# Optimization experiments

Hardware: AMD Instinct MI355X
Metric: run time of the kernel (lower is better)

Reference implementation:

```python
import jax, jax.numpy as jnp
import numpy as np

EPS = 1e-5

def layer_norm(x, g, b):
    m = jnp.mean(x, axis=-1, keepdims=True)
    v = jnp.var(x, axis=-1, keepdims=True)
    return (x - m) / jnp.sqrt(v + EPS) * g + b


def setup_inputs() -> dict:
    key = jax.random.key(0)
    ks = jax.random.split(key, 12)
    B, L, D = 4, 4096, 512
    DF = 2 * D  # dim * dim_ff_scale
    inp = {
        "x": jax.random.normal(ks[0], (B, L, D), dtype=jnp.float32),
        "hidden_real": jax.random.normal(ks[1], (B, D), dtype=jnp.float32),
        "hidden_imag": jax.random.normal(ks[2], (B, D), dtype=jnp.float32),
        # SpiralConv complex params (real/imag parts), as torch.randn cfloat
        "phazor_re": jax.random.normal(ks[3], (D,), dtype=jnp.float32),
        "phazor_im": jax.random.normal(ks[4], (D,), dtype=jnp.float32),
        "pinit_re": jax.random.normal(ks[5], (D,), dtype=jnp.float32),
        "pinit_im": jax.random.normal(ks[6], (D,), dtype=jnp.float32),
        # shared LayerNorm params
        "ln_g": jnp.ones((D,), dtype=jnp.float32),
        "ln_b": jnp.zeros((D,), dtype=jnp.float32),
        # FFN params
        "w1": jax.random.normal(ks[7], (D, DF), dtype=jnp.float32) * (1.0 / np.sqrt(D)),
        "b1": jnp.zeros((DF,), dtype=jnp.float32),
        "w2": jax.random.normal(ks[8], (DF, D), dtype=jnp.float32) * (1.0 / np.sqrt(DF)),
        "b2": jnp.zeros((D,), dtype=jnp.float32),
    }
    return inp


def reference(x, hidden_real, hidden_imag, phazor_re, phazor_im,
              pinit_re, pinit_im, ln_g, ln_b, w1, b1, w2, b2):
    B, L, D = x.shape
    p = jax.lax.complex(phazor_re, phazor_im)
    pinit = jax.lax.complex(pinit_re, pinit_im)
    hidden_last = jax.lax.complex(hidden_real, hidden_imag)

    # phazor = p/|p| * exp(-|p|)  (unit direction, decaying magnitude)
    absp = jnp.abs(p)
    phazor = p / absp * jnp.exp(-absp)

    # phazor_progression[t, d] = phazor[d] ** t
    t = jnp.arange(L, dtype=jnp.float32)
    prog = jnp.exp(t[:, None] * jnp.log(phazor)[None, :])  # [L, D] complex
    filt = prog * pinit[None, :]                            # [L, D]

    x_res = x
    xn = layer_norm(x, ln_g, ln_b)

    # FFT long convolution along sequence, zero-padded to 2L (linear conv)
    filt_fft = jnp.fft.fft(filt, n=2 * L, axis=0)           # [2L, D]
    x_fft = jnp.fft.fft(xn, n=2 * L, axis=1)                # [B, 2L, D]
    conv = jnp.fft.ifft(filt_fft[None, :, :] * x_fft, axis=1)[:, :L, :]

    hidden = conv + hidden_last[:, None, :] * prog[None, :, :] * phazor[None, None, :]

    y = hidden.real + x_res
    yn = layer_norm(y, ln_g, ln_b)
    h = yn @ w1 + b1
    h = h * jax.nn.sigmoid(h)  # SiLU; dropout=0 (eval) is identity
    out = h @ w2 + b2 + y
    return out, hidden
```

## Files before the change

kernel.cpp:

```cpp
#include <hip/hip_runtime.h>
#include <hip/hip_bf16.h>
#include <math.h>

#define BB 4
#define LL 4096
#define DD 512
#define DF 1024
#define CHUNKS 64
#define LC 64
#define HALF_ROWS 8192

typedef __bf16 bf16x8 __attribute__((ext_vector_type(8)));
typedef float f32x4 __attribute__((ext_vector_type(4)));

__device__ inline void get_phazor(const float* __restrict__ pre, const float* __restrict__ pim,
                                  int d, float& ar, float& ai) {
    float pr = pre[d], pi = pim[d];
    float ab = sqrtf(pr * pr + pi * pi);
    float sc = expf(-ab) / ab;
    ar = pr * sc;
    ai = pi * sc;
}

__global__ __launch_bounds__(256) void k_wt(const float* __restrict__ w1, const float* __restrict__ w2,
                                            __bf16* __restrict__ w1t, __bf16* __restrict__ w2t) {
    __shared__ float tile[32][33];
    const float* src;
    __bf16* dst;
    int R, C;
    if (blockIdx.y == 0) { src = w1; dst = w1t; R = DD; C = DF; }
    else                 { src = w2; dst = w2t; R = DF; C = DD; }
    int ntx = C / 32;
    int c0 = (blockIdx.x % ntx) * 32, r0 = (blockIdx.x / ntx) * 32;
    int tx = threadIdx.x & 31, ty = threadIdx.x >> 5;
#pragma unroll
    for (int i = 0; i < 32; i += 8)
        tile[ty + i][tx] = src[(size_t)(r0 + ty + i) * C + c0 + tx];
    __syncthreads();
#pragma unroll
    for (int i = 0; i < 32; i += 8)
        dst[(size_t)(c0 + ty + i) * R + r0 + tx] = (__bf16)tile[tx][ty + i];
}

__global__ __launch_bounds__(256) void k_xstats(const float* __restrict__ x, float* __restrict__ xstats) {
    int wave = threadIdx.x >> 6, lane = threadIdx.x & 63;
    size_t row = (size_t)blockIdx.x * 4 + wave;
    const float4* xr = reinterpret_cast<const float4*>(x + row * DD) + lane * 2;
    float4 a = xr[0], b = xr[1];
    float s = a.x + a.y + a.z + a.w + b.x + b.y + b.z + b.w;
    float q = a.x * a.x + a.y * a.y + a.z * a.z + a.w * a.w +
              b.x * b.x + b.y * b.y + b.z * b.z + b.w * b.w;
#pragma unroll
    for (int off = 32; off; off >>= 1) {
        s += __shfl_down(s, off);
        q += __shfl_down(q, off);
    }
    if (lane == 0) {
        float m = s * (1.0f / DD);
        float v = q * (1.0f / DD) - m * m;
        xstats[row * 2 + 0] = m;
        xstats[row * 2 + 1] = rsqrtf(v + 1e-5f);
    }
}

__global__ __launch_bounds__(512) void k_scan_partial(
    const float* __restrict__ x, const float* __restrict__ xstats,
    const float* __restrict__ pre, const float* __restrict__ pim,
    const float* __restrict__ pinr, const float* __restrict__ pini,
    const float* __restrict__ g, const float* __restrict__ bvec,
    float* __restrict__ carry) {
    int d = threadIdx.x;
    int c = blockIdx.x % CHUNKS, b = blockIdx.x / CHUNKS;
    float ar, ai;
    get_phazor(pre, pim, d, ar, ai);
    float pr = pinr[d], pi = pini[d];
    float gd = g[d], bd = bvec[d];
    float hr = 0.f, hi = 0.f;
    int l0 = c * LC;
    const float* xp = x + ((size_t)b * LL + l0) * DD + d;
    const float* st = xstats + ((size_t)b * LL + l0) * 2;
    for (int i = 0; i < LC; i++) {
        float m = st[2 * i], r = st[2 * i + 1];
        float xn = (xp[(size_t)i * DD] - m) * r * gd + bd;
        float ur = pr * xn, ui = pi * xn;
        float t = ar * hr - ai * hi + ur;
        hi = ar * hi + ai * hr + ui;
        hr = t;
    }
    size_t idx = ((size_t)blockIdx.x * DD + d) * 2;
    carry[idx] = hr;
    carry[idx + 1] = hi;
}

__global__ __launch_bounds__(512) void k_chunk_scan(
    const float* __restrict__ hr0, const float* __restrict__ hi0,
    const float* __restrict__ pre, const float* __restrict__ pim,
    const float* __restrict__ carry, float* __restrict__ carry_in) {
    int d = threadIdx.x, b = blockIdx.x;
    float ar, ai;
    get_phazor(pre, pim, d, ar, ai);
    float sr = ar, si = ai;
#pragma unroll
    for (int i = 0; i < 6; i++) {
        float t = sr * sr - si * si;
        si = 2.f * sr * si;
        sr = t;
    }
    float cr = hr0[b * DD + d], ci = hi0[b * DD + d];
    for (int k = 0; k < CHUNKS; k++) {
        size_t idx = (((size_t)b * CHUNKS + k) * DD + d) * 2;
        carry_in[idx] = cr;
        carry_in[idx + 1] = ci;
        float tr = carry[idx], ti = carry[idx + 1];
        float t = sr * cr - si * ci + tr;
        ci = sr * ci + si * cr + ti;
        cr = t;
    }
}

template <int MODE>
__global__ __launch_bounds__(512) void k_scan_out(
    const float* __restrict__ x, const float* __restrict__ xstats,
    const float* __restrict__ pre, const float* __restrict__ pim,
    const float* __restrict__ pinr, const float* __restrict__ pini,
    const float* __restrict__ g, const float* __restrict__ bvec,
    const float* __restrict__ carry_in,
    float* __restrict__ out_y, float* __restrict__ hid) {
    int d = threadIdx.x;
    int c = blockIdx.x % CHUNKS, b = blockIdx.x / CHUNKS;
    float ar, ai;
    get_phazor(pre, pim, d, ar, ai);
    float pr = pinr[d], pi = pini[d];
    float gd = g[d], bd = bvec[d];
    size_t cidx = ((size_t)blockIdx.x * DD + d) * 2;
    float hr = carry_in[cidx], hi = carry_in[cidx + 1];
    int l0 = c * LC;
    const float* xp = x + ((size_t)b * LL + l0) * DD + d;
    const float* st = xstats + ((size_t)b * LL + l0) * 2;
    for (int i = 0; i < LC; i++) {
        float m = st[2 * i], r = st[2 * i + 1];
        float xv = xp[(size_t)i * DD];
        float xn = (xv - m) * r * gd + bd;
        float ur = pr * xn, ui = pi * xn;
        float t = ar * hr - ai * hi + ur;
        hi = ar * hi + ai * hr + ui;
        hr = t;
        size_t row = (size_t)b * LL + l0 + i;
        if constexpr (MODE == 0) {
            out_y[row * DD + d] = hr + xv;
        } else if constexpr (MODE == 1) {
            hid[row * DD + d] = hr;
        } else if constexpr (MODE == 2) {
            reinterpret_cast<float2*>(hid)[row * DD + d] = make_float2(hr, hi);
        } else {
            out_y[row * DD + d] = hr + xv;
            hid[row * DD + d] = hr;
        }
    }
}

__global__ __launch_bounds__(256) void k_ynorm(const float* __restrict__ y,
                                               const float* __restrict__ g, const float* __restrict__ bvec,
                                               __bf16* __restrict__ yn) {
    int wave = threadIdx.x >> 6, lane = threadIdx.x & 63;
    size_t row = (size_t)blockIdx.x * 4 + wave;
    const float4* yr = reinterpret_cast<const float4*>(y + row * DD) + lane * 2;
    float4 a = yr[0], b = yr[1];
    float s = a.x + a.y + a.z + a.w + b.x + b.y + b.z + b.w;
    float q = a.x * a.x + a.y * a.y + a.z * a.z + a.w * a.w +
              b.x * b.x + b.y * b.y + b.z * b.z + b.w * b.w;
#pragma unroll
    for (int off = 32; off; off >>= 1) {
        s += __shfl_xor(s, off);
        q += __shfl_xor(q, off);
    }
    float m = s * (1.0f / DD);
    float r = rsqrtf(q * (1.0f / DD) - m * m + 1e-5f);
    int dbase = lane * 8;
    const float4* gp = reinterpret_cast<const float4*>(g + dbase);
    const float4* bp = reinterpret_cast<const float4*>(bvec + dbase);
    float4 g0 = gp[0], g1 = gp[1], b0 = bp[0], b1 = bp[1];
    bf16x8 o;
    o[0] = (__bf16)((a.x - m) * r * g0.x + b0.x);
    o[1] = (__bf16)((a.y - m) * r * g0.y + b0.y);
    o[2] = (__bf16)((a.z - m) * r * g0.z + b0.z);
    o[3] = (__bf16)((a.w - m) * r * g0.w + b0.w);
    o[4] = (__bf16)((b.x - m) * r * g1.x + b1.x);
    o[5] = (__bf16)((b.y - m) * r * g1.y + b1.y);
    o[6] = (__bf16)((b.z - m) * r * g1.z + b1.z);
    o[7] = (__bf16)((b.w - m) * r * g1.w + b1.w);
    *reinterpret_cast<bf16x8*>(yn + row * DD + dbase) = o;
}

template <int BM, int BN, int KDIM, int NDIM, int EPI>
__global__ __launch_bounds__(512) void k_gemm(
    const __bf16* __restrict__ A, const __bf16* __restrict__ Bt,
    const float* __restrict__ bias, const float* __restrict__ yadd,
    float* __restrict__ outf, __bf16* __restrict__ outb) {
    __shared__ __align__(16) __bf16 As[2][BM * 64];
    __shared__ __align__(16) __bf16 Bs[2][BN * 64];
    constexpr int NT = NDIM / BN;
    constexpr int MR = BM / 32;
    constexpr int NR = BN / 64;
    constexpr int LPT = BM / 64 + BN / 64;
    int nwg = gridDim.x;
    int bid = blockIdx.x;
    int swz = (bid & 7) * (nwg >> 3) + (bid >> 3);
    int m0 = (swz / NT) * BM;
    int n0 = (swz % NT) * BN;
    int tid = threadIdx.x;
    int wid = tid >> 6, lane = tid & 63;

    f32x4 acc[MR][NR] = {};

    int wm = (wid >> 2) * (BM / 2), wn = (wid & 3) * (BN / 4);
    int fr = lane & 15;
    int qbase = lane >> 4;

    auto stage = [&](int buf, int k0) {
#pragma unroll
        for (int i = 0; i < BM / 64; i++) {
            int c = tid + i * 512;
            int row = c >> 3, kq = c & 7;
            int kqg = kq ^ (row & 7);
            const __bf16* ga = A + (size_t)(m0 + row) * KDIM + k0 + kqg * 8;
            __bf16* la = &As[buf][(size_t)(i * 512 + wid * 64) * 8];
            __builtin_amdgcn_global_load_lds((const __attribute__((address_space(1))) unsigned int*)ga,
                                             (__attribute__((address_space(3))) unsigned int*)la, 16, 0, 0);
        }
#pragma unroll
        for (int i = 0; i < BN / 64; i++) {
            int c = tid + i * 512;
            int row = c >> 3, kq = c & 7;
            int kqg = kq ^ (row & 7);
            const __bf16* gb = Bt + (size_t)(n0 + row) * KDIM + k0 + kqg * 8;
            __bf16* lb = &Bs[buf][(size_t)(i * 512 + wid * 64) * 8];
            __builtin_amdgcn_global_load_lds((const __attribute__((address_space(1))) unsigned int*)gb,
                                             (__attribute__((address_space(3))) unsigned int*)lb, 16, 0, 0);
        }
    };

    auto compute = [&](int buf) {
#pragma unroll
        for (int ks = 0; ks < 2; ks++) {
            int q = ks * 4 + qbase;
            bf16x8 af[MR], bfv[NR];
#pragma unroll
            for (int mi = 0; mi < MR; mi++) {
                int R = wm + mi * 16 + fr;
                af[mi] = *reinterpret_cast<const bf16x8*>(&As[buf][R * 64 + ((q ^ (R & 7)) << 3)]);
            }
#pragma unroll
            for (int ni = 0; ni < NR; ni++) {
                int R = wn + ni * 16 + fr;
                bfv[ni] = *reinterpret_cast<const bf16x8*>(&Bs[buf][R * 64 + ((q ^ (R & 7)) << 3)]);
            }
            __builtin_amdgcn_s_setprio(1);
#pragma unroll
            for (int mi = 0; mi < MR; mi++)
#pragma unroll
                for (int ni = 0; ni < NR; ni++)
                    acc[mi][ni] = __builtin_amdgcn_mfma_f32_16x16x32_bf16(af[mi], bfv[ni],
                                                                          acc[mi][ni], 0, 0, 0);
            __builtin_amdgcn_s_setprio(0);
        }
    };

    stage(0, 0);
    int cur = 0;
    for (int k0 = 64; k0 < KDIM; k0 += 64) {
        stage(cur ^ 1, k0);
        asm volatile("s_waitcnt vmcnt(%0)" ::"i"(LPT) : "memory");
        __builtin_amdgcn_s_barrier();
        compute(cur);
        __builtin_amdgcn_s_barrier();
        cur ^= 1;
    }
    asm volatile("s_waitcnt vmcnt(0)" ::: "memory");
    __builtin_amdgcn_s_barrier();
    compute(cur);

    int orow = (lane >> 4) * 4;
    int ocol = lane & 15;
#pragma unroll
    for (int mi = 0; mi < MR; mi++) {
#pragma unroll
        for (int ni = 0; ni < NR; ni++) {
            int gr = m0 + wm + mi * 16 + orow;
            int gc = n0 + wn + ni * 16 + ocol;
            float bv = bias[gc];
#pragma unroll
            for (int j = 0; j < 4; j++) {
                float v = acc[mi][ni][j] + bv;
                size_t idx = (size_t)(gr + j) * NDIM + gc;
                if constexpr (EPI == 1) {
                    float sv = v / (1.0f + __expf(-v));
                    outb[idx] = (__bf16)sv;
                } else {
                    outf[idx] = v + yadd[idx];
                }
            }
        }
    }
}

extern "C" void kernel_launch(void* const* d_in, const int* in_sizes, int n_in,
                              void* d_out, int out_size, void* d_ws, size_t ws_size,
                              hipStream_t stream) {
    const float* x = (const float*)d_in[0];
    const float* hr0 = (const float*)d_in[1];
    const float* hi0 = (const float*)d_in[2];
    const float* pre = (const float*)d_in[3];
    const float* pim = (const float*)d_in[4];
    const float* pinr = (const float*)d_in[5];
    const float* pini = (const float*)d_in[6];
    const float* lng = (const float*)d_in[7];
    const float* lnb = (const float*)d_in[8];
    const float* w1 = (const float*)d_in[9];
    const float* b1 = (const float*)d_in[10];
    const float* w2 = (const float*)d_in[11];
    const float* b2 = (const float*)d_in[12];

    const size_t n = (size_t)BB * LL * DD;
    float* outp = (float*)d_out;
    char* hidbase = (char*)d_out + n * 4;
    float* hidp = (float*)hidbase;
    bool interleaved = (out_size >= (int)(3 * n));

    char* ws = (char*)d_ws;
    float* xstats = (float*)ws;      ws += (size_t)BB * LL * 2 * 4;
    float* carry = (float*)ws;       ws += (size_t)BB * CHUNKS * DD * 8;
    float* carry_in = (float*)ws;    ws += (size_t)BB * CHUNKS * DD * 8;
    __bf16* w1t = (__bf16*)ws;       ws += (size_t)DD * DF * 2;
    __bf16* w2t = (__bf16*)ws;       ws += (size_t)DF * DD * 2;
    char* ws_big = ws;
    const size_t SMALL = (size_t)(128 + 1024 + 1024 + 1024 + 1024) * 1024;
    const size_t NEED_FULL = SMALL + ((size_t)48 << 20);
    const size_t NEED_HALF = SMALL + ((size_t)24 << 20);

    k_wt<<<dim3((DD / 32) * (DF / 32), 2), 256, 0, stream>>>(w1, w2, w1t, w2t);
    k_xstats<<<(BB * LL) / 4, 256, 0, stream>>>(x, xstats);
    k_scan_partial<<<BB * CHUNKS, 512, 0, stream>>>(x, xstats, pre, pim, pinr, pini, lng, lnb, carry);
    k_chunk_scan<<<BB, 512, 0, stream>>>(hr0, hi0, pre, pim, carry, carry_in);

    if (!interleaved && ws_size >= NEED_FULL) {
        __bf16* yn = (__bf16*)ws_big;
        __bf16* h1 = (__bf16*)(ws_big + ((size_t)16 << 20));
        k_scan_out<3><<<BB * CHUNKS, 512, 0, stream>>>(x, xstats, pre, pim, pinr, pini, lng, lnb,
                                                       carry_in, outp, hidp);
        k_ynorm<<<(BB * LL) / 4, 256, 0, stream>>>(outp, lng, lnb, yn);
        k_gemm<256, 256, DD, DF, 1><<<(BB * LL / 256) * (DF / 256), 512, 0, stream>>>(
            yn, w1t, b1, nullptr, nullptr, h1);
        k_gemm<128, 256, DF, DD, 2><<<(BB * LL / 128) * (DD / 256), 512, 0, stream>>>(
            h1, w2t, b2, outp, outp, nullptr);
    } else if (!interleaved && ws_size >= NEED_HALF) {
        __bf16* yn_h = (__bf16*)ws_big;
        __bf16* h1_h = (__bf16*)(ws_big + ((size_t)8 << 20));
        k_scan_out<3><<<BB * CHUNKS, 512, 0, stream>>>(x, xstats, pre, pim, pinr, pini, lng, lnb,
                                                       carry_in, outp, hidp);
        for (int h = 0; h < 2; h++) {
            float* yh = outp + (size_t)h * HALF_ROWS * DD;
            k_ynorm<<<HALF_ROWS / 4, 256, 0, stream>>>(yh, lng, lnb, yn_h);
            k_gemm<256, 256, DD, DF, 1><<<(HALF_ROWS / 256) * (DF / 256), 512, 0, stream>>>(
                yn_h, w1t, b1, nullptr, nullptr, h1_h);
            k_gemm<128, 256, DF, DD, 2><<<(HALF_ROWS / 128) * (DD / 256), 512, 0, stream>>>(
                h1_h, w2t, b2, yh, yh, nullptr);
        }
    } else {
        __bf16* yn_h = (__bf16*)hidbase;
        __bf16* h1_h = (__bf16*)(hidbase + ((size_t)8 << 20));
        k_scan_out<0><<<BB * CHUNKS, 512, 0, stream>>>(x, xstats, pre, pim, pinr, pini, lng, lnb,
                                                       carry_in, outp, nullptr);
        for (int h = 0; h < 2; h++) {
            float* yh = outp + (size_t)h * HALF_ROWS * DD;
            k_ynorm<<<HALF_ROWS / 4, 256, 0, stream>>>(yh, lng, lnb, yn_h);
            k_gemm<256, 256, DD, DF, 1><<<(HALF_ROWS / 256) * (DF / 256), 512, 0, stream>>>(
                yn_h, w1t, b1, nullptr, nullptr, h1_h);
            k_gemm<128, 256, DF, DD, 2><<<(HALF_ROWS / 128) * (DD / 256), 512, 0, stream>>>(
                h1_h, w2t, b2, yh, yh, nullptr);
        }
        if (interleaved) {
            k_scan_out<2><<<BB * CHUNKS, 512, 0, stream>>>(x, xstats, pre, pim, pinr, pini, lng, lnb,
                                                           carry_in, nullptr, hidp);
        } else {
            k_scan_out<1><<<BB * CHUNKS, 512, 0, stream>>>(x, xstats, pre, pim, pinr, pini, lng, lnb,
                                                           carry_in, nullptr, hidp);
        }
    }
}
```

Before: 113.5 us.

## Fuse layernorm stats and y-norm into wave-per-row chunked scan kernels

Removes the separate x-stats kernel by computing row mean and rstd inside the scan kernels: each 64-lane wave owns a full row, and each lane handles 8 channels with float4 loads. The output scan kernel also computes the y layernorm and writes the bf16 yn directly, dropping the k_ynorm pass when workspace is large enough. Chunk count goes up to 256 with one wave per block, and the carry is updated in place instead of being copied to a second buffer. Each lane now keeps many more values in registers, and the recurrence per chunk is shorter but there are more chunks to combine serially.

```diff
diff --git a/kernel.cpp b/kernel.cpp
--- a/kernel.cpp
+++ b/kernel.cpp
@@ -6,8 +6,6 @@
 #define LL 4096
 #define DD 512
 #define DF 1024
-#define CHUNKS 64
-#define LC 64
 #define HALF_ROWS 8192
 
 typedef __bf16 bf16x8 __attribute__((ext_vector_type(8)));
@@ -42,120 +40,156 @@
         dst[(size_t)(c0 + ty + i) * R + r0 + tx] = (__bf16)tile[tx][ty + i];
 }
 
-__global__ __launch_bounds__(256) void k_xstats(const float* __restrict__ x, float* __restrict__ xstats) {
-    int wave = threadIdx.x >> 6, lane = threadIdx.x & 63;
-    size_t row = (size_t)blockIdx.x * 4 + wave;
-    const float4* xr = reinterpret_cast<const float4*>(x + row * DD) + lane * 2;
-    float4 a = xr[0], b = xr[1];
-    float s = a.x + a.y + a.z + a.w + b.x + b.y + b.z + b.w;
-    float q = a.x * a.x + a.y * a.y + a.z * a.z + a.w * a.w +
-              b.x * b.x + b.y * b.y + b.z * b.z + b.w * b.w;
-#pragma unroll
-    for (int off = 32; off; off >>= 1) {
-        s += __shfl_down(s, off);
-        q += __shfl_down(q, off);
-    }
-    if (lane == 0) {
-        float m = s * (1.0f / DD);
-        float v = q * (1.0f / DD) - m * m;
-        xstats[row * 2 + 0] = m;
-        xstats[row * 2 + 1] = rsqrtf(v + 1e-5f);
-    }
-}
-
-__global__ __launch_bounds__(512) void k_scan_partial(
-    const float* __restrict__ x, const float* __restrict__ xstats,
+template <int NCH>
+__global__ __launch_bounds__(64) void k_scan_partial(
+    const float* __restrict__ x,
     const float* __restrict__ pre, const float* __restrict__ pim,
     const float* __restrict__ pinr, const float* __restrict__ pini,
     const float* __restrict__ g, const float* __restrict__ bvec,
     float* __restrict__ carry) {
-    int d = threadIdx.x;
-    int c = blockIdx.x % CHUNKS, b = blockIdx.x / CHUNKS;
-    float ar, ai;
-    get_phazor(pre, pim, d, ar, ai);
-    float pr = pinr[d], pi = pini[d];
-    float gd = g[d], bd = bvec[d];
-    float hr = 0.f, hi = 0.f;
-    int l0 = c * LC;
-    const float* xp = x + ((size_t)b * LL + l0) * DD + d;
-    const float* st = xstats + ((size_t)b * LL + l0) * 2;
-    for (int i = 0; i < LC; i++) {
-        float m = st[2 * i], r = st[2 * i + 1];
-        float xn = (xp[(size_t)i * DD] - m) * r * gd + bd;
-        float ur = pr * xn, ui = pi * xn;
-        float t = ar * hr - ai * hi + ur;
-        hi = ar * hi + ai * hr + ui;
-        hr = t;
-    }
-    size_t idx = ((size_t)blockIdx.x * DD + d) * 2;
-    carry[idx] = hr;
-    carry[idx + 1] = hi;
-}
-
-__global__ __launch_bounds__(512) void k_chunk_scan(
+    constexpr int LCC = LL / NCH;
+    int b = blockIdx.x / NCH, c = blockIdx.x % NCH;
+    int lane = threadIdx.x;
+    int d0 = lane * 8;
+    float ar[8], ai[8], pr[8], pi[8], gd[8], bd[8], hr[8], hi[8];
+#pragma unroll
+    for (int j = 0; j < 8; j++) {
+        get_phazor(pre, pim, d0 + j, ar[j], ai[j]);
+        pr[j] = pinr[d0 + j]; pi[j] = pini[d0 + j];
+        gd[j] = g[d0 + j];    bd[j] = bvec[d0 + j];
+        hr[j] = 0.f; hi[j] = 0.f;
+    }
+    const float* xrow = x + ((size_t)b * LL + (size_t)c * LCC) * DD + d0;
+#pragma unroll 4
+    for (int i = 0; i < LCC; i++) {
+        float4 xa = *reinterpret_cast<const float4*>(xrow);
+        float4 xb = *reinterpret_cast<const float4*>(xrow + 4);
+        float xv[8] = {xa.x, xa.y, xa.z, xa.w, xb.x, xb.y, xb.z, xb.w};
+        float s = 0.f, q = 0.f;
+#pragma unroll
+        for (int j = 0; j < 8; j++) { s += xv[j]; q += xv[j] * xv[j]; }
+#pragma unroll
+        for (int off = 32; off; off >>= 1) { s += __shfl_xor(s, off); q += __shfl_xor(q, off); }
+        float m = s * (1.0f / DD);
+        float r = rsqrtf(q * (1.0f / DD) - m * m + 1e-5f);
+#pragma unroll
+        for (int j = 0; j < 8; j++) {
+            float xn = (xv[j] - m) * r * gd[j] + bd[j];
+            float t = ar[j] * hr[j] - ai[j] * hi[j] + pr[j] * xn;
+            hi[j] = ar[j] * hi[j] + ai[j] * hr[j] + pi[j] * xn;
+            hr[j] = t;
+        }
+        xrow += DD;
+    }
+    float2* cp = reinterpret_cast<float2*>(carry) + (size_t)blockIdx.x * DD + d0;
+#pragma unroll
+    for (int j = 0; j < 8; j++) cp[j] = make_float2(hr[j], hi[j]);
+}
+
+template <int NCH>
+__global__ __launch_bounds__(64) void k_chunk_scan(
     const float* __restrict__ hr0, const float* __restrict__ hi0,
     const float* __restrict__ pre, const float* __restrict__ pim,
-    const float* __restrict__ carry, float* __restrict__ carry_in) {
-    int d = threadIdx.x, b = blockIdx.x;
+    float* __restrict__ carry) {
+    constexpr int LCC = LL / NCH;
+    int b = blockIdx.x >> 3;
+    int d = ((blockIdx.x & 7) << 6) + threadIdx.x;
     float ar, ai;
     get_phazor(pre, pim, d, ar, ai);
     float sr = ar, si = ai;
 #pragma unroll
-    for (int i = 0; i < 6; i++) {
+    for (int p = 1; p < LCC; p <<= 1) {
         float t = sr * sr - si * si;
         si = 2.f * sr * si;
         sr = t;
     }
     float cr = hr0[b * DD + d], ci = hi0[b * DD + d];
-    for (int k = 0; k < CHUNKS; k++) {
-        size_t idx = (((size_t)b * CHUNKS + k) * DD + d) * 2;
-        carry_in[idx] = cr;
-        carry_in[idx + 1] = ci;
-        float tr = carry[idx], ti = carry[idx + 1];
-        float t = sr * cr - si * ci + tr;
-        ci = sr * ci + si * cr + ti;
+    float2* cp = reinterpret_cast<float2*>(carry);
+    for (int k = 0; k < NCH; k++) {
+        size_t idx = ((size_t)b * NCH + k) * DD + d;
+        float2 t2 = cp[idx];
+        cp[idx] = make_float2(cr, ci);
+        float t = sr * cr - si * ci + t2.x;
+        ci = sr * ci + si * cr + t2.y;
         cr = t;
     }
 }
 
-template <int MODE>
-__global__ __launch_bounds__(512) void k_scan_out(
-    const float* __restrict__ x, const float* __restrict__ xstats,
+template <int NCH, int MODE>
+__global__ __launch_bounds__(64) void k_scan_out(
+    const float* __restrict__ x,
     const float* __restrict__ pre, const float* __restrict__ pim,
     const float* __restrict__ pinr, const float* __restrict__ pini,
     const float* __restrict__ g, const float* __restrict__ bvec,
-    const float* __restrict__ carry_in,
-    float* __restrict__ out_y, float* __restrict__ hid) {
-    int d = threadIdx.x;
-    int c = blockIdx.x % CHUNKS, b = blockIdx.x / CHUNKS;
-    float ar, ai;
-    get_phazor(pre, pim, d, ar, ai);
-    float pr = pinr[d], pi = pini[d];
-    float gd = g[d], bd = bvec[d];
-    size_t cidx = ((size_t)blockIdx.x * DD + d) * 2;
-    float hr = carry_in[cidx], hi = carry_in[cidx + 1];
-    int l0 = c * LC;
-    const float* xp = x + ((size_t)b * LL + l0) * DD + d;
-    const float* st = xstats + ((size_t)b * LL + l0) * 2;
-    for (int i = 0; i < LC; i++) {
-        float m = st[2 * i], r = st[2 * i + 1];
-        float xv = xp[(size_t)i * DD];
-        float xn = (xv - m) * r * gd + bd;
-        float ur = pr * xn, ui = pi * xn;
-        float t = ar * hr - ai * hi + ur;
-        hi = ar * hi + ai * hr + ui;
-        hr = t;
-        size_t row = (size_t)b * LL + l0 + i;
-        if constexpr (MODE == 0) {
-            out_y[row * DD + d] = hr + xv;
-        } else if constexpr (MODE == 1) {
-            hid[row * DD + d] = hr;
-        } else if constexpr (MODE == 2) {
-            reinterpret_cast<float2*>(hid)[row * DD + d] = make_float2(hr, hi);
-        } else {
-            out_y[row * DD + d] = hr + xv;
-            hid[row * DD + d] = hr;
-        }
+    const float* __restrict__ carry,
+    float* __restrict__ out_y, float* __restrict__ hid, __bf16* __restrict__ yn) {
+    constexpr int LCC = LL / NCH;
+    int b = blockIdx.x / NCH, c = blockIdx.x % NCH;
+    int lane = threadIdx.x;
+    int d0 = lane * 8;
+    float ar[8], ai[8], pr[8], pi[8], gd[8], bd[8], hr[8], hi[8];
+    const float2* cp = reinterpret_cast<const float2*>(carry) + (size_t)blockIdx.x * DD + d0;
+#pragma unroll
+    for (int j = 0; j < 8; j++) {
+        get_phazor(pre, pim, d0 + j, ar[j], ai[j]);
+        pr[j] = pinr[d0 + j]; pi[j] = pini[d0 + j];
+        gd[j] = g[d0 + j];    bd[j] = bvec[d0 + j];
+        float2 cj = cp[j];
+        hr[j] = cj.x; hi[j] = cj.y;
+    }
+    size_t row0 = (size_t)b * LL + (size_t)c * LCC;
+    const float* xrow = x + row0 * DD + d0;
+#pragma unroll 4
+    for (int i = 0; i < LCC; i++) {
+        float4 xa = *reinterpret_cast<const float4*>(xrow);
+        float4 xb = *reinterpret_cast<const float4*>(xrow + 4);
+        float xv[8] = {xa.x, xa.y, xa.z, xa.w, xb.x, xb.y, xb.z, xb.w};
+        float s = 0.f, q = 0.f;
+#pragma unroll
+        for (int j = 0; j < 8; j++) { s += xv[j]; q += xv[j] * xv[j]; }
+#pragma unroll
+        for (int off = 32; off; off >>= 1) { s += __shfl_xor(s, off); q += __shfl_xor(q, off); }
+        float m = s * (1.0f / DD);
+        float r = rsqrtf(q * (1.0f / DD) - m * m + 1e-5f);
+        float y[8];
+#pragma unroll
+        for (int j = 0; j < 8; j++) {
+            float xn = (xv[j] - m) * r * gd[j] + bd[j];
+            float t = ar[j] * hr[j] - ai[j] * hi[j] + pr[j] * xn;
+            hi[j] = ar[j] * hi[j] + ai[j] * hr[j] + pi[j] * xn;
+            hr[j] = t;
+            y[j] = hr[j] + xv[j];
+        }
+        size_t row = row0 + i;
+        if constexpr (MODE == 0 || MODE == 3 || MODE == 4) {
+            float4* yp = reinterpret_cast<float4*>(out_y + row * DD + d0);
+            yp[0] = make_float4(y[0], y[1], y[2], y[3]);
+            yp[1] = make_float4(y[4], y[5], y[6], y[7]);
+        }
+        if constexpr (MODE == 1 || MODE == 3 || MODE == 4) {
+            float4* hp = reinterpret_cast<float4*>(hid + row * DD + d0);
+            hp[0] = make_float4(hr[0], hr[1], hr[2], hr[3]);
+            hp[1] = make_float4(hr[4], hr[5], hr[6], hr[7]);
+        }
+        if constexpr (MODE == 2) {
+            float2* hp = reinterpret_cast<float2*>(hid) + row * DD + d0;
+#pragma unroll
+            for (int j = 0; j < 8; j++) hp[j] = make_float2(hr[j], hi[j]);
+        }
+        if constexpr (MODE == 4) {
+            float ys = 0.f, yq = 0.f;
+#pragma unroll
+            for (int j = 0; j < 8; j++) { ys += y[j]; yq += y[j] * y[j]; }
+#pragma unroll
+            for (int off = 32; off; off >>= 1) { ys += __shfl_xor(ys, off); yq += __shfl_xor(yq, off); }
+            float ym = ys * (1.0f / DD);
+            float yr = rsqrtf(yq * (1.0f / DD) - ym * ym + 1e-5f);
+            bf16x8 o;
+#pragma unroll
+            for (int j = 0; j < 8; j++) o[j] = (__bf16)((y[j] - ym) * yr * gd[j] + bd[j]);
+            *reinterpret_cast<bf16x8*>(yn + row * DD + d0) = o;
+        }
+        xrow += DD;
     }
 }
 
@@ -322,42 +356,60 @@
     const float* b2 = (const float*)d_in[12];
 
     const size_t n = (size_t)BB * LL * DD;
+    const size_t MB1 = 1ull << 20;
     float* outp = (float*)d_out;
     char* hidbase = (char*)d_out + n * 4;
     float* hidp = (float*)hidbase;
     bool interleaved = (out_size >= (int)(3 * n));
 
+    const size_t CARRY256 = (size_t)BB * 256 * DD * 8;
+    const size_t CARRY64 = (size_t)BB * 64 * DD * 8;
+    const size_t WB = 2 * MB1;
+
     char* ws = (char*)d_ws;
-    float* xstats = (float*)ws;      ws += (size_t)BB * LL * 2 * 4;
-    float* carry = (float*)ws;       ws += (size_t)BB * CHUNKS * DD * 8;
-    float* carry_in = (float*)ws;    ws += (size_t)BB * CHUNKS * DD * 8;
-    __bf16* w1t = (__bf16*)ws;       ws += (size_t)DD * DF * 2;
-    __bf16* w2t = (__bf16*)ws;       ws += (size_t)DF * DD * 2;
-    char* ws_big = ws;
-    const size_t SMALL = (size_t)(128 + 1024 + 1024 + 1024 + 1024) * 1024;
-    const size_t NEED_FULL = SMALL + ((size_t)48 << 20);
-    const size_t NEED_HALF = SMALL + ((size_t)24 << 20);
-
-    k_wt<<<dim3((DD / 32) * (DF / 32), 2), 256, 0, stream>>>(w1, w2, w1t, w2t);
-    k_xstats<<<(BB * LL) / 4, 256, 0, stream>>>(x, xstats);
-    k_scan_partial<<<BB * CHUNKS, 512, 0, stream>>>(x, xstats, pre, pim, pinr, pini, lng, lnb, carry);
-    k_chunk_scan<<<BB, 512, 0, stream>>>(hr0, hi0, pre, pim, carry, carry_in);
-
-    if (!interleaved && ws_size >= NEED_FULL) {
-        __bf16* yn = (__bf16*)ws_big;
-        __bf16* h1 = (__bf16*)(ws_big + ((size_t)16 << 20));
-        k_scan_out<3><<<BB * CHUNKS, 512, 0, stream>>>(x, xstats, pre, pim, pinr, pini, lng, lnb,
-                                                       carry_in, outp, hidp);
-        k_ynorm<<<(BB * LL) / 4, 256, 0, stream>>>(outp, lng, lnb, yn);
+
+    k_wt<<<dim3((DD / 32) * (DF / 32), 2), 256, 0, stream>>>(
+        w1, w2, (__bf16*)(ws + ((ws_size >= CARRY256 + WB + 48 * MB1 && !interleaved) ? CARRY256 : CARRY64)),
+        (__bf16*)(ws + ((ws_size >= CARRY256 + WB + 48 * MB1 && !interleaved) ? CARRY256 : CARRY64) + MB1));
+
+    if (!interleaved && ws_size >= CARRY256 + WB + 48 * MB1) {
+        float* carry = (float*)ws;
+        __bf16* w1t = (__bf16*)(ws + CARRY256);
+        __bf16* w2t = (__bf16*)(ws + CARRY256 + MB1);
+        __bf16* yn = (__bf16*)(ws + CARRY256 + WB);
+        __bf16* h1 = (__bf16*)(ws + CARRY256 + WB + 16 * MB1);
+        k_scan_partial<256><<<BB * 256, 64, 0, stream>>>(x, pre, pim, pinr, pini, lng, lnb, carry);
+        k_chunk_scan<256><<<BB * 8, 64, 0, stream>>>(hr0, hi0, pre, pim, carry);
+        k_scan_out<256, 4><<<BB * 256, 64, 0, stream>>>(x, pre, pim, pinr, pini, lng, lnb,
+                                                        carry, outp, hidp, yn);
         k_gemm<256, 256, DD, DF, 1><<<(BB * LL / 256) * (DF / 256), 512, 0, stream>>>(
             yn, w1t, b1, nullptr, nullptr, h1);
         k_gemm<128, 256, DF, DD, 2><<<(BB * LL / 128) * (DD / 256), 512, 0, stream>>>(
             h1, w2t, b2, outp, outp, nullptr);
-    } else if (!interleaved && ws_size >= NEED_HALF) {
-        __bf16* yn_h = (__bf16*)ws_big;
-        __bf16* h1_h = (__bf16*)(ws_big + ((size_t)8 << 20));
-        k_scan_out<3><<<BB * CHUNKS, 512, 0, stream>>>(x, xstats, pre, pim, pinr, pini, lng, lnb,
-                                                       carry_in, outp, hidp);
+    } else if (!interleaved && ws_size >= CARRY64 + WB + 48 * MB1) {
+        float* carry = (float*)ws;
+        __bf16* w1t = (__bf16*)(ws + CARRY64);
+        __bf16* w2t = (__bf16*)(ws + CARRY64 + MB1);
+        __bf16* yn = (__bf16*)(ws + CARRY64 + WB);
+        __bf16* h1 = (__bf16*)(ws + CARRY64 + WB + 16 * MB1);
+        k_scan_partial<64><<<BB * 64, 64, 0, stream>>>(x, pre, pim, pinr, pini, lng, lnb, carry);
+        k_chunk_scan<64><<<BB * 8, 64, 0, stream>>>(hr0, hi0, pre, pim, carry);
+        k_scan_out<64, 4><<<BB * 64, 64, 0, stream>>>(x, pre, pim, pinr, pini, lng, lnb,
+                                                      carry, outp, hidp, yn);
+        k_gemm<256, 256, DD, DF, 1><<<(BB * LL / 256) * (DF / 256), 512, 0, stream>>>(
+            yn, w1t, b1, nullptr, nullptr, h1);
+        k_gemm<128, 256, DF, DD, 2><<<(BB * LL / 128) * (DD / 256), 512, 0, stream>>>(
+            h1, w2t, b2, outp, outp, nullptr);
+    } else if (!interleaved && ws_size >= CARRY64 + WB + 24 * MB1) {
+        float* carry = (float*)ws;
+        __bf16* w1t = (__bf16*)(ws + CARRY64);
+        __bf16* w2t = (__bf16*)(ws + CARRY64 + MB1);
+        __bf16* yn_h = (__bf16*)(ws + CARRY64 + WB);
+        __bf16* h1_h = (__bf16*)(ws + CARRY64 + WB + 8 * MB1);
+        k_scan_partial<64><<<BB * 64, 64, 0, stream>>>(x, pre, pim, pinr, pini, lng, lnb, carry);
+        k_chunk_scan<64><<<BB * 8, 64, 0, stream>>>(hr0, hi0, pre, pim, carry);
+        k_scan_out<64, 3><<<BB * 64, 64, 0, stream>>>(x, pre, pim, pinr, pini, lng, lnb,
+                                                      carry, outp, hidp, nullptr);
         for (int h = 0; h < 2; h++) {
             float* yh = outp + (size_t)h * HALF_ROWS * DD;
             k_ynorm<<<HALF_ROWS / 4, 256, 0, stream>>>(yh, lng, lnb, yn_h);
@@ -367,10 +419,15 @@
                 h1_h, w2t, b2, yh, yh, nullptr);
         }
     } else {
+        float* carry = (float*)ws;
+        __bf16* w1t = (__bf16*)(ws + CARRY64);
+        __bf16* w2t = (__bf16*)(ws + CARRY64 + MB1);
         __bf16* yn_h = (__bf16*)hidbase;
-        __bf16* h1_h = (__bf16*)(hidbase + ((size_t)8 << 20));
-        k_scan_out<0><<<BB * CHUNKS, 512, 0, stream>>>(x, xstats, pre, pim, pinr, pini, lng, lnb,
-                                                       carry_in, outp, nullptr);
+        __bf16* h1_h = (__bf16*)(hidbase + 8 * MB1);
+        k_scan_partial<64><<<BB * 64, 64, 0, stream>>>(x, pre, pim, pinr, pini, lng, lnb, carry);
+        k_chunk_scan<64><<<BB * 8, 64, 0, stream>>>(hr0, hi0, pre, pim, carry);
+        k_scan_out<64, 0><<<BB * 64, 64, 0, stream>>>(x, pre, pim, pinr, pini, lng, lnb,
+                                                      carry, outp, nullptr, nullptr);
         for (int h = 0; h < 2; h++) {
             float* yh = outp + (size_t)h * HALF_ROWS * DD;
             k_ynorm<<<HALF_ROWS / 4, 256, 0, stream>>>(yh, lng, lnb, yn_h);
@@ -380,11 +437,11 @@
                 h1_h, w2t, b2, yh, yh, nullptr);
         }
         if (interleaved) {
-            k_scan_out<2><<<BB * CHUNKS, 512, 0, stream>>>(x, xstats, pre, pim, pinr, pini, lng, lnb,
-                                                           carry_in, nullptr, hidp);
+            k_scan_out<64, 2><<<BB * 64, 64, 0, stream>>>(x, pre, pim, pinr, pini, lng, lnb,
+                                                          carry, nullptr, hidp, nullptr);
         } else {
-            k_scan_out<1><<<BB * CHUNKS, 512, 0, stream>>>(x, xstats, pre, pim, pinr, pini, lng, lnb,
-                                                           carry_in, nullptr, hidp);
-        }
-    }
-}
+            k_scan_out<64, 1><<<BB * 64, 64, 0, stream>>>(x, pre, pim, pinr, pini, lng, lnb,
+                                                          carry, nullptr, hidp, nullptr);
+        }
+    }
+}
```

Result: slower. 121.4 us (+7.0%).

## Split GEMM K-tile staging into half-slices and interleave with MFMA compute

Applied to the files above, without the earlier changes.

The bf16 GEMM now stages each 64-wide K tile as two 32-wide slices in a k-quad-major LDS layout instead of a row-major XOR-swizzled layout. The second slice's global-to-LDS load is issued between the two compute halves, and the waitcnt thresholds are tightened per slice. The goal is finer overlap of memory traffic with MFMA work and simpler, conflict-free LDS reads without the swizzle. The cost is an extra barrier per K step and a more delicate accounting of outstanding loads.

```diff
diff --git a/kernel.cpp b/kernel.cpp
--- a/kernel.cpp
+++ b/kernel.cpp
@@ -202,7 +202,10 @@
     constexpr int NT = NDIM / BN;
     constexpr int MR = BM / 32;
     constexpr int NR = BN / 64;
-    constexpr int LPT = BM / 64 + BN / 64;
+    constexpr int SLA = BM / 128, SLB = BN / 128;
+    constexpr int SPL = SLA + SLB;
+    constexpr int LOGA = (BM == 256 ? 8 : 7);
+    constexpr int LOGB = (BN == 256 ? 8 : 7);
     int nwg = gridDim.x;
     int bid = blockIdx.x;
     int swz = (bid & 7) * (nwg >> 3) + (bid >> 3);
@@ -217,68 +220,72 @@
     int fr = lane & 15;
     int qbase = lane >> 4;
 
-    auto stage = [&](int buf, int k0) {
-#pragma unroll
-        for (int i = 0; i < BM / 64; i++) {
-            int c = tid + i * 512;
-            int row = c >> 3, kq = c & 7;
-            int kqg = kq ^ (row & 7);
-            const __bf16* ga = A + (size_t)(m0 + row) * KDIM + k0 + kqg * 8;
-            __bf16* la = &As[buf][(size_t)(i * 512 + wid * 64) * 8];
+    auto stage_slice = [&](int buf, int k0, int s) {
+#pragma unroll
+        for (int j = 0; j < SLA; j++) {
+            int lc = tid + j * 512;
+            int row = lc & (BM - 1);
+            int kq = s * 4 + (lc >> LOGA);
+            const __bf16* ga = A + (size_t)(m0 + row) * KDIM + k0 + kq * 8;
+            __bf16* la = &As[buf][(size_t)(s * BM * 4 + j * 512 + wid * 64) * 8];
             __builtin_amdgcn_global_load_lds((const __attribute__((address_space(1))) unsigned int*)ga,
                                              (__attribute__((address_space(3))) unsigned int*)la, 16, 0, 0);
         }
 #pragma unroll
-        for (int i = 0; i < BN / 64; i++) {
-            int c = tid + i * 512;
-            int row = c >> 3, kq = c & 7;
-            int kqg = kq ^ (row & 7);
-            const __bf16* gb = Bt + (size_t)(n0 + row) * KDIM + k0 + kqg * 8;
-            __bf16* lb = &Bs[buf][(size_t)(i * 512 + wid * 64) * 8];
+        for (int j = 0; j < SLB; j++) {
+            int lc = tid + j * 512;
+            int row = lc & (BN - 1);
+            int kq = s * 4 + (lc >> LOGB);
+            const __bf16* gb = Bt + (size_t)(n0 + row) * KDIM + k0 + kq * 8;
+            __bf16* lb = &Bs[buf][(size_t)(s * BN * 4 + j * 512 + wid * 64) * 8];
             __builtin_amdgcn_global_load_lds((const __attribute__((address_space(1))) unsigned int*)gb,
                                              (__attribute__((address_space(3))) unsigned int*)lb, 16, 0, 0);
         }
     };
 
-    auto compute = [&](int buf) {
-#pragma unroll
-        for (int ks = 0; ks < 2; ks++) {
-            int q = ks * 4 + qbase;
-            bf16x8 af[MR], bfv[NR];
-#pragma unroll
-            for (int mi = 0; mi < MR; mi++) {
-                int R = wm + mi * 16 + fr;
-                af[mi] = *reinterpret_cast<const bf16x8*>(&As[buf][R * 64 + ((q ^ (R & 7)) << 3)]);
-            }
-#pragma unroll
-            for (int ni = 0; ni < NR; ni++) {
-                int R = wn + ni * 16 + fr;
-                bfv[ni] = *reinterpret_cast<const bf16x8*>(&Bs[buf][R * 64 + ((q ^ (R & 7)) << 3)]);
-            }
-            __builtin_amdgcn_s_setprio(1);
-#pragma unroll
-            for (int mi = 0; mi < MR; mi++)
-#pragma unroll
-                for (int ni = 0; ni < NR; ni++)
-                    acc[mi][ni] = __builtin_amdgcn_mfma_f32_16x16x32_bf16(af[mi], bfv[ni],
-                                                                          acc[mi][ni], 0, 0, 0);
-            __builtin_amdgcn_s_setprio(0);
-        }
+    auto compute_ks = [&](int buf, int ks) {
+        int q = ks * 4 + qbase;
+        bf16x8 af[MR], bfv[NR];
+#pragma unroll
+        for (int mi = 0; mi < MR; mi++) {
+            int R = wm + mi * 16 + fr;
+            af[mi] = *reinterpret_cast<const bf16x8*>(&As[buf][((size_t)q * BM + R) * 8]);
+        }
+#pragma unroll
+        for (int ni = 0; ni < NR; ni++) {
+            int R = wn + ni * 16 + fr;
+            bfv[ni] = *reinterpret_cast<const bf16x8*>(&Bs[buf][((size_t)q * BN + R) * 8]);
+        }
+        __builtin_amdgcn_s_setprio(1);
+#pragma unroll
+        for (int mi = 0; mi < MR; mi++)
+#pragma unroll
+            for (int ni = 0; ni < NR; ni++)
+                acc[mi][ni] = __builtin_amdgcn_mfma_f32_16x16x32_bf16(af[mi], bfv[ni],
+                                                                      acc[mi][ni], 0, 0, 0);
+        __builtin_amdgcn_s_setprio(0);
     };
 
-    stage(0, 0);
+    stage_slice(0, 0, 0);
+    stage_slice(0, 0, 1);
     int cur = 0;
     for (int k0 = 64; k0 < KDIM; k0 += 64) {
-        stage(cur ^ 1, k0);
-        asm volatile("s_waitcnt vmcnt(%0)" ::"i"(LPT) : "memory");
+        stage_slice(cur ^ 1, k0, 0);
+        asm volatile("s_waitcnt vmcnt(%0)" ::"i"(2 * SPL) : "memory");
         __builtin_amdgcn_s_barrier();
-        compute(cur);
+        compute_ks(cur, 0);
+        stage_slice(cur ^ 1, k0, 1);
+        asm volatile("s_waitcnt vmcnt(%0)" ::"i"(2 * SPL) : "memory");
         __builtin_amdgcn_s_barrier();
+        compute_ks(cur, 1);
         cur ^= 1;
     }
+    asm volatile("s_waitcnt vmcnt(%0)" ::"i"(SPL) : "memory");
+    __builtin_amdgcn_s_barrier();
+    compute_ks(cur, 0);
     asm volatile("s_waitcnt vmcnt(0)" ::: "memory");
     __builtin_amdgcn_s_barrier();
-    compute(cur);
+    compute_ks(cur, 1);
 
     int orow = (lane >> 4) * 4;
     int ocol = lane & 15;
```

Result: slower. 129.7 us (+14.4%).

## Double scan chunks, split chunk-scan across blocks, and reuse carry buffer in place

Applied to the files above, without the earlier changes.

Halves the chunk length and doubles the chunk count, so the partial-scan and scan-out kernels launch 512 blocks with shorter serial loops. The inter-chunk carry scan is spread over 32 blocks of 64 threads instead of 4 blocks of 512, with float2 loads and stores. Carry-ins now overwrite the carry buffer in place, which removes the separate carry_in array. The cost is a longer serial carry-propagation loop (128 steps) and more carry traffic.

```diff
diff --git a/kernel.cpp b/kernel.cpp
--- a/kernel.cpp
+++ b/kernel.cpp
@@ -6,8 +6,8 @@
 #define LL 4096
 #define DD 512
 #define DF 1024
-#define CHUNKS 64
-#define LC 64
+#define CHUNKS 128
+#define LC 32
 #define HALF_ROWS 8192
 
 typedef __bf16 bf16x8 __attribute__((ext_vector_type(8)));
@@ -92,28 +92,29 @@
     carry[idx + 1] = hi;
 }
 
-__global__ __launch_bounds__(512) void k_chunk_scan(
+__global__ __launch_bounds__(64) void k_chunk_scan(
     const float* __restrict__ hr0, const float* __restrict__ hi0,
     const float* __restrict__ pre, const float* __restrict__ pim,
-    const float* __restrict__ carry, float* __restrict__ carry_in) {
-    int d = threadIdx.x, b = blockIdx.x;
+    float* __restrict__ carry) {
+    int b = blockIdx.x >> 3;
+    int d = ((blockIdx.x & 7) << 6) + threadIdx.x;
     float ar, ai;
     get_phazor(pre, pim, d, ar, ai);
     float sr = ar, si = ai;
 #pragma unroll
-    for (int i = 0; i < 6; i++) {
+    for (int p = 1; p < LC; p <<= 1) {
         float t = sr * sr - si * si;
         si = 2.f * sr * si;
         sr = t;
     }
     float cr = hr0[b * DD + d], ci = hi0[b * DD + d];
+    float2* cp = reinterpret_cast<float2*>(carry);
     for (int k = 0; k < CHUNKS; k++) {
-        size_t idx = (((size_t)b * CHUNKS + k) * DD + d) * 2;
-        carry_in[idx] = cr;
-        carry_in[idx + 1] = ci;
-        float tr = carry[idx], ti = carry[idx + 1];
-        float t = sr * cr - si * ci + tr;
-        ci = sr * ci + si * cr + ti;
+        size_t idx = ((size_t)b * CHUNKS + k) * DD + d;
+        float2 t2 = cp[idx];
+        cp[idx] = make_float2(cr, ci);
+        float t = sr * cr - si * ci + t2.x;
+        ci = sr * ci + si * cr + t2.y;
         cr = t;
     }
 }
@@ -330,24 +331,23 @@
     char* ws = (char*)d_ws;
     float* xstats = (float*)ws;      ws += (size_t)BB * LL * 2 * 4;
     float* carry = (float*)ws;       ws += (size_t)BB * CHUNKS * DD * 8;
-    float* carry_in = (float*)ws;    ws += (size_t)BB * CHUNKS * DD * 8;
     __bf16* w1t = (__bf16*)ws;       ws += (size_t)DD * DF * 2;
     __bf16* w2t = (__bf16*)ws;       ws += (size_t)DF * DD * 2;
     char* ws_big = ws;
-    const size_t SMALL = (size_t)(128 + 1024 + 1024 + 1024 + 1024) * 1024;
+    const size_t SMALL = ((size_t)128 << 10) + ((size_t)2 << 20) + ((size_t)2 << 20);
     const size_t NEED_FULL = SMALL + ((size_t)48 << 20);
     const size_t NEED_HALF = SMALL + ((size_t)24 << 20);
 
     k_wt<<<dim3((DD / 32) * (DF / 32), 2), 256, 0, stream>>>(w1, w2, w1t, w2t);
     k_xstats<<<(BB * LL) / 4, 256, 0, stream>>>(x, xstats);
     k_scan_partial<<<BB * CHUNKS, 512, 0, stream>>>(x, xstats, pre, pim, pinr, pini, lng, lnb, carry);
-    k_chunk_scan<<<BB, 512, 0, stream>>>(hr0, hi0, pre, pim, carry, carry_in);
+    k_chunk_scan<<<BB * 8, 64, 0, stream>>>(hr0, hi0, pre, pim, carry);
 
     if (!interleaved && ws_size >= NEED_FULL) {
         __bf16* yn = (__bf16*)ws_big;
         __bf16* h1 = (__bf16*)(ws_big + ((size_t)16 << 20));
         k_scan_out<3><<<BB * CHUNKS, 512, 0, stream>>>(x, xstats, pre, pim, pinr, pini, lng, lnb,
-                                                       carry_in, outp, hidp);
+                                                       carry, outp, hidp);
         k_ynorm<<<(BB * LL) / 4, 256, 0, stream>>>(outp, lng, lnb, yn);
         k_gemm<256, 256, DD, DF, 1><<<(BB * LL / 256) * (DF / 256), 512, 0, stream>>>(
             yn, w1t, b1, nullptr, nullptr, h1);
@@ -357,7 +357,7 @@
         __bf16* yn_h = (__bf16*)ws_big;
         __bf16* h1_h = (__bf16*)(ws_big + ((size_t)8 << 20));
         k_scan_out<3><<<BB * CHUNKS, 512, 0, stream>>>(x, xstats, pre, pim, pinr, pini, lng, lnb,
-                                                       carry_in, outp, hidp);
+                                                       carry, outp, hidp);
         for (int h = 0; h < 2; h++) {
             float* yh = outp + (size_t)h * HALF_ROWS * DD;
             k_ynorm<<<HALF_ROWS / 4, 256, 0, stream>>>(yh, lng, lnb, yn_h);
@@ -370,7 +370,7 @@
         __bf16* yn_h = (__bf16*)hidbase;
         __bf16* h1_h = (__bf16*)(hidbase + ((size_t)8 << 20));
         k_scan_out<0><<<BB * CHUNKS, 512, 0, stream>>>(x, xstats, pre, pim, pinr, pini, lng, lnb,
-                                                       carry_in, outp, nullptr);
+                                                       carry, outp, nullptr);
         for (int h = 0; h < 2; h++) {
             float* yh = outp + (size_t)h * HALF_ROWS * DD;
             k_ynorm<<<HALF_ROWS / 4, 256, 0, stream>>>(yh, lng, lnb, yn_h);
@@ -381,10 +381,10 @@
         }
         if (interleaved) {
             k_scan_out<2><<<BB * CHUNKS, 512, 0, stream>>>(x, xstats, pre, pim, pinr, pini, lng, lnb,
-                                                           carry_in, nullptr, hidp);
+                                                           carry, nullptr, hidp);
         } else {
             k_scan_out<1><<<BB * CHUNKS, 512, 0, stream>>>(x, xstats, pre, pim, pinr, pini, lng, lnb,
-                                                           carry_in, nullptr, hidp);
-        }
-    }
-}
+                                                           carry, nullptr, hidp);
+        }
+    }
+}
```

Result: no change. 114.6 us (+1.1%).
